# Kernel optimization log

Measured on AMD Instinct MI355X. Metric: run time of the kernel, lower is better.

## Reference

```python
import jax, jax.numpy as jnp
import numpy as np

B, T, F_IN = 64, 512, 264        # batch, time, total features
NONLSTM = 8                      # trailing non-LSTM feature channels
F_LSTM = F_IN - NONLSTM          # 256 features fed to the LSTM stack
HIDDEN = [512, 512]              # stacked OptimizedLSTMCell dims
DENSE = [512, 256]
PRED, FPP = 16, 4                # predictions, features_per_prediction


def _glorot(key, shape):
    fan_in, fan_out = shape[0], shape[1]
    lim = jnp.sqrt(6.0 / (fan_in + fan_out))
    return jax.random.uniform(key, shape, jnp.float32, -lim, lim)


def setup_inputs() -> dict:
    key = jax.random.key(0)
    ks = jax.random.split(key, 16)
    inp = {"x": jax.random.normal(ks[0], (B, T, F_IN), jnp.float32)}
    # LSTM layer params: Wi [in,4H] (no bias on input proj), Wh [H,4H], b [4H]
    in_dim = F_LSTM
    for j, h in enumerate(HIDDEN):
        inp[f"Wi{j}"] = _glorot(ks[1 + 3 * j], (in_dim, 4 * h))
        inp[f"Wh{j}"] = _glorot(ks[2 + 3 * j], (h, 4 * h))
        inp[f"b{j}"] = jnp.zeros((4 * h,), jnp.float32)
        in_dim = h
    # Dense head
    d_in = HIDDEN[-1] + NONLSTM
    for i, d in enumerate(DENSE):
        inp[f"Wd{i}"] = _glorot(ks[8 + 2 * i], (d_in, d))
        inp[f"bd{i}"] = jnp.zeros((d,), jnp.float32)
        d_in = d
    inp["Wf"] = _glorot(ks[14], (d_in, PRED * FPP))
    inp["bf"] = jnp.zeros((PRED * FPP,), jnp.float32)
    return inp


def lstm_layer(x, Wi, Wh, b):
    """flax OptimizedLSTMCell scanned over time. x: [B, T, F] -> [B, T, H]."""
    Bq = x.shape[0]
    H = Wh.shape[0]
    xw = jnp.einsum('btf,fg->btg', x, Wi)  # precompute input projections

    def step(carry, z_in):
        c, h = carry
        z = z_in + h @ Wh + b
        i, f, g, o = jnp.split(z, 4, axis=-1)
        c = jax.nn.sigmoid(f) * c + jax.nn.sigmoid(i) * jnp.tanh(g)
        h = jax.nn.sigmoid(o) * jnp.tanh(c)
        return (c, h), h

    c0 = jnp.zeros((Bq, H), x.dtype)
    h0 = jnp.zeros((Bq, H), x.dtype)
    _, hs = jax.lax.scan(step, (c0, h0), jnp.swapaxes(xw, 0, 1))
    return jnp.swapaxes(hs, 0, 1)


def reference(x, Wi0, Wh0, b0, Wi1, Wh1, b1, Wd0, bd0, Wd1, bd1, Wf, bf):
    last_features = x[:, -1, -NONLSTM:]          # [B, 8]
    h = x[:, :, :-NONLSTM]                       # [B, T, 256]
    # single LSTM branch: history == T, downsample == 1
    h = lstm_layer(h, Wi0, Wh0, b0)
    h = lstm_layer(h, Wi1, Wh1, b1)
    out = h[:, -1, :]                            # [B, H]
    out = jnp.concatenate([out, last_features], axis=1)
    out = jax.nn.relu(out @ Wd0 + bd0)
    out = jax.nn.relu(out @ Wd1 + bd1)
    out = out @ Wf + bf
    out = out.reshape((-1, PRED, FPP))
    return jax.nn.sigmoid(out)
```

## Files before the change

### kernel.cpp

```cpp
#include <hip/hip_runtime.h>
#include <hip/hip_bf16.h>

typedef __hip_bfloat16 bf16;
typedef short bf16x8 __attribute__((ext_vector_type(8)));
typedef float f32x4 __attribute__((ext_vector_type(4)));
typedef unsigned long long u64;
typedef unsigned int u32;

#define MFMA16(A, B, C) __builtin_amdgcn_mfma_f32_16x16x32_bf16(A, B, C, 0, 0, 0)

__device__ __forceinline__ float sigf(float x) { return 1.f / (1.f + __expf(-x)); }
__device__ __forceinline__ float tanh_fast(float x) { return 2.f / (1.f + __expf(-2.f * x)) - 1.f; }

__device__ __forceinline__ bf16x8 ld16(const u64* p) {
  u64 lo = __hip_atomic_load(p, __ATOMIC_RELAXED, __HIP_MEMORY_SCOPE_SYSTEM);
  u64 hi = __hip_atomic_load(p + 1, __ATOMIC_RELAXED, __HIP_MEMORY_SCOPE_SYSTEM);
  union { u64 q[2]; bf16x8 v; } u;
  u.q[0] = lo; u.q[1] = hi;
  return u.v;
}

__global__ __launch_bounds__(256) void transpose_k(const float* __restrict__ W,
                                                   bf16* __restrict__ WT,
                                                   int K, int N) {
  __shared__ bf16 tile[32][33];
  const int n0 = blockIdx.x * 32, k0 = blockIdx.y * 32;
  const int c = threadIdx.x & 31, r0 = threadIdx.x >> 5;
  for (int i = 0; i < 4; ++i) {
    int r = r0 + 8 * i;
    tile[r][c] = __float2bfloat16(W[(long)(k0 + r) * N + (n0 + c)]);
  }
  __syncthreads();
  for (int i = 0; i < 4; ++i) {
    int r = r0 + 8 * i;
    WT[(long)(n0 + r) * K + (k0 + c)] = tile[c][r];
  }
}

__device__ __forceinline__ void gather16(const u64* __restrict__ mat, int m, int q,
                                         bf16x8* out) {
#pragma unroll
  for (int i = 0; i < 16; ++i) {
    const int s = i * 4 + q;
    out[i] = ld16(mat + ((long)(s << 6) + m) * 2);
  }
}

__global__ __launch_bounds__(256, 1) void lstm2_fused_k(
    const float* __restrict__ x,
    const bf16* __restrict__ WiT0, const bf16* __restrict__ WhT0,
    const float* __restrict__ bias0,
    const bf16* __restrict__ WiT1, const bf16* __restrict__ WhT1,
    const float* __restrict__ bias1,
    u64* __restrict__ h1D, u64* __restrict__ h2D,
    u32* __restrict__ sent)
{
  __shared__ short Wis[32 * 520];
  __shared__ short Whs[32 * 520];
  __shared__ float zs[32 * 66];
  __shared__ __align__(16) bf16 hstage[64 * 8];

  const int layer = blockIdx.x >> 6;
  const int w = blockIdx.x & 63;
  const int tid = threadIdx.x;
  const int lane = tid & 63;
  const int wv = tid >> 6;
  const int q = lane >> 4;
  const int r = lane & 15;

  const int K_in = layer ? 512 : 256;
  const bf16* WiT = layer ? WiT1 : WiT0;
  const bf16* WhT = layer ? WhT1 : WhT0;
  const float* bias = layer ? bias1 : bias0;
  u32* s0 = sent;
  u32* s1 = sent + 512 * 64;
  u64* hprevD = layer ? h2D : h1D;
  u64* houtD = layer ? h2D : h1D;
  u32* smy = (layer ? s1 : s0);

  for (int idx = tid; idx < 32 * 64; idx += 256) {
    const int j = idx >> 6, kc = idx & 63;
    const int zc = (j >> 3) * 512 + w * 8 + (j & 7);
    *(bf16x8*)(Whs + j * 520 + kc * 8) = *(const bf16x8*)(WhT + (long)zc * 512 + kc * 8);
  }
  const int csh = layer ? 6 : 5;
  const int cmask = (1 << csh) - 1;
  for (int idx = tid; idx < (32 << csh); idx += 256) {
    const int j = idx >> csh, kc = idx & cmask;
    const int zc = (j >> 3) * 512 + w * 8 + (j & 7);
    *(bf16x8*)(Wis + j * 520 + kc * 8) = *(const bf16x8*)(WiT + (long)zc * K_in + kc * 8);
  }

  const int m = wv * 16 + r;
  const short* wi0p = Wis + r * 520;
  const short* wi1p = Wis + (16 + r) * 520;
  const short* wh0p = Whs + r * 520;
  const short* wh1p = Whs + (16 + r) * 520;

  const int gb = tid & 63;
  const int gc0 = tid >> 6;
  float bias_r[2][4];
  for (int s = 0; s < 2; ++s)
    for (int g = 0; g < 4; ++g)
      bias_r[s][g] = bias[g * 512 + w * 8 + gc0 + 4 * s];
  float creg[2] = {0.f, 0.f};

  __syncthreads();

  for (int t = 0; t < 512; ++t) {
    f32x4 acc0 = {0.f, 0.f, 0.f, 0.f};
    f32x4 acc1 = {0.f, 0.f, 0.f, 0.f};

    if (layer == 0) {
      bf16x8 ax[8];
      const float* row = x + ((long)m * 512 + t) * 264;
#pragma unroll
      for (int i = 0; i < 8; ++i) {
        const float4 f0 = *(const float4*)(row + i * 32 + q * 8);
        const float4 f1 = *(const float4*)(row + i * 32 + q * 8 + 4);
        union { short s[8]; bf16x8 v8; } o;
        o.s[0] = __builtin_bit_cast(short, __float2bfloat16(f0.x));
        o.s[1] = __builtin_bit_cast(short, __float2bfloat16(f0.y));
        o.s[2] = __builtin_bit_cast(short, __float2bfloat16(f0.z));
        o.s[3] = __builtin_bit_cast(short, __float2bfloat16(f0.w));
        o.s[4] = __builtin_bit_cast(short, __float2bfloat16(f1.x));
        o.s[5] = __builtin_bit_cast(short, __float2bfloat16(f1.y));
        o.s[6] = __builtin_bit_cast(short, __float2bfloat16(f1.z));
        o.s[7] = __builtin_bit_cast(short, __float2bfloat16(f1.w));
        ax[i] = o.v8;
      }
#pragma unroll
      for (int i = 0; i < 8; ++i) {
        const int kk = i * 32;
        acc0 = MFMA16(ax[i], *(const bf16x8*)(wi0p + kk + q * 8), acc0);
        acc1 = MFMA16(ax[i], *(const bf16x8*)(wi1p + kk + q * 8), acc1);
      }
      if (t > 0) {
        if (tid < 64) {
          const u32* sp = s0 + (t - 1) * 64 + tid;
          while (__ballot(__hip_atomic_load(sp, __ATOMIC_RELAXED,
                                            __HIP_MEMORY_SCOPE_SYSTEM) != 0) != ~0ull)
            __builtin_amdgcn_s_sleep(2);
        }
        __syncthreads();
        bf16x8 ah[16];
        gather16(h1D + (long)(t - 1) * 8192, m, q, ah);
#pragma unroll
        for (int i = 0; i < 16; ++i) {
          const int kk = i * 32;
          acc0 = MFMA16(ah[i], *(const bf16x8*)(wh0p + kk + q * 8), acc0);
          acc1 = MFMA16(ah[i], *(const bf16x8*)(wh1p + kk + q * 8), acc1);
        }
      }
    } else {
      if (tid < 64) {
        const u32* sp = s0 + t * 64 + tid;
        while (__ballot(__hip_atomic_load(sp, __ATOMIC_RELAXED,
                                          __HIP_MEMORY_SCOPE_SYSTEM) != 0) != ~0ull)
          __builtin_amdgcn_s_sleep(2);
      }
      __syncthreads();
      bf16x8 ax[16];
      gather16(h1D + (long)t * 8192, m, q, ax);
#pragma unroll
      for (int i = 0; i < 16; ++i) {
        const int kk = i * 32;
        acc0 = MFMA16(ax[i], *(const bf16x8*)(wi0p + kk + q * 8), acc0);
        acc1 = MFMA16(ax[i], *(const bf16x8*)(wi1p + kk + q * 8), acc1);
      }
      if (t > 0) {
        if (tid < 64) {
          const u32* sp = s1 + (t - 1) * 64 + tid;
          while (__ballot(__hip_atomic_load(sp, __ATOMIC_RELAXED,
                                            __HIP_MEMORY_SCOPE_SYSTEM) != 0) != ~0ull)
            __builtin_amdgcn_s_sleep(2);
        }
        __syncthreads();
        bf16x8 ah[16];
        gather16(h2D + (long)(t - 1) * 8192, m, q, ah);
#pragma unroll
        for (int i = 0; i < 16; ++i) {
          const int kk = i * 32;
          acc0 = MFMA16(ah[i], *(const bf16x8*)(wh0p + kk + q * 8), acc0);
          acc1 = MFMA16(ah[i], *(const bf16x8*)(wh1p + kk + q * 8), acc1);
        }
      }
    }

    {
      const int brow = wv * 16 + q * 4;
      for (int i = 0; i < 4; ++i) zs[r * 66 + brow + i] = acc0[i];
      for (int i = 0; i < 4; ++i) zs[(16 + r) * 66 + brow + i] = acc1[i];
    }
    __syncthreads();

    for (int s = 0; s < 2; ++s) {
      const int c = gc0 + 4 * s;
      const float zi = zs[(c)*66 + gb] + bias_r[s][0];
      const float zf = zs[(8 + c) * 66 + gb] + bias_r[s][1];
      const float zg = zs[(16 + c) * 66 + gb] + bias_r[s][2];
      const float zo = zs[(24 + c) * 66 + gb] + bias_r[s][3];
      const float cnew = sigf(zf) * creg[s] + sigf(zi) * tanh_fast(zg);
      const float hnew = sigf(zo) * tanh_fast(cnew);
      creg[s] = cnew;
      hstage[gb * 8 + c] = __float2bfloat16(hnew);
    }
    __syncthreads();

    if (tid < 64) {
      const u64* src = (const u64*)(hstage + tid * 8);
      u64* dst = houtD + (((long)t * 64 + w) * 64 + tid) * 2;
      __hip_atomic_store(dst, src[0], __ATOMIC_RELAXED, __HIP_MEMORY_SCOPE_SYSTEM);
      __hip_atomic_store(dst + 1, src[1], __ATOMIC_RELAXED, __HIP_MEMORY_SCOPE_SYSTEM);
    }
    if (tid == 0)
      __hip_atomic_store(smy + t * 64 + w, 1u, __ATOMIC_RELEASE, __HIP_MEMORY_SCOPE_AGENT);
  }
}

__global__ __launch_bounds__(256) void head_k(
    const u64* __restrict__ h2D,
    const float* __restrict__ x,
    const float* __restrict__ Wd0, const float* __restrict__ bd0,
    const float* __restrict__ Wd1, const float* __restrict__ bd1,
    const float* __restrict__ Wf, const float* __restrict__ bfv,
    float* __restrict__ out) {
  const int b = blockIdx.x, tid = threadIdx.x;
  __shared__ float in0[520];
  __shared__ float d0s[512];
  __shared__ float d1s[256];
  if (tid < 64) {
    const int s = tid;
    bf16x8 v = ld16(h2D + (((long)511 * 64 + s) * 64 + b) * 2);
    union { bf16x8 v8; short sh[8]; } u;
    u.v8 = v;
    for (int j = 0; j < 8; ++j)
      in0[s * 8 + j] = __bfloat162float(__builtin_bit_cast(bf16, u.sh[j]));
  }
  if (tid < 8) in0[512 + tid] = x[((long)(b * 512 + 511)) * 264 + 256 + tid];
  __syncthreads();
  for (int j = tid; j < 512; j += 256) {
    float a = bd0[j];
    for (int k = 0; k < 520; ++k) a += in0[k] * Wd0[(long)k * 512 + j];
    d0s[j] = fmaxf(a, 0.f);
  }
  __syncthreads();
  if (tid < 256) {
    const int j = tid;
    float a = bd1[j];
    for (int k = 0; k < 512; ++k) a += d0s[k] * Wd1[(long)k * 256 + j];
    d1s[j] = fmaxf(a, 0.f);
  }
  __syncthreads();
  if (tid < 64) {
    const int j = tid;
    float a = bfv[j];
    for (int k = 0; k < 256; ++k) a += d1s[k] * Wf[(long)k * 64 + j];
    out[b * 64 + j] = sigf(a);
  }
}

extern "C" void kernel_launch(void* const* d_in, const int* in_sizes, int n_in,
                              void* d_out, int out_size, void* d_ws, size_t ws_size,
                              hipStream_t stream) {
  const float* x   = (const float*)d_in[0];
  const float* Wi0 = (const float*)d_in[1];
  const float* Wh0 = (const float*)d_in[2];
  const float* b0  = (const float*)d_in[3];
  const float* Wi1 = (const float*)d_in[4];
  const float* Wh1 = (const float*)d_in[5];
  const float* b1  = (const float*)d_in[6];
  const float* Wd0 = (const float*)d_in[7];
  const float* bd0 = (const float*)d_in[8];
  const float* Wd1 = (const float*)d_in[9];
  const float* bd1 = (const float*)d_in[10];
  const float* Wf  = (const float*)d_in[11];
  const float* bf_ = (const float*)d_in[12];
  float* out = (float*)d_out;

  char* ws = (char*)d_ws;
  size_t off = 0;
  auto carve = [&](size_t bytes) {
    void* p = ws + off;
    off += (bytes + 255) & ~(size_t)255;
    return p;
  };
  u32* sent = (u32*)carve((size_t)2 * 512 * 64 * 4);
  const size_t zero_bytes = off;
  bf16* WiT0 = (bf16*)carve((size_t)2048 * 256 * 2);
  bf16* WhT0 = (bf16*)carve((size_t)2048 * 512 * 2);
  bf16* WiT1 = (bf16*)carve((size_t)2048 * 512 * 2);
  bf16* WhT1 = (bf16*)carve((size_t)2048 * 512 * 2);
  u64*  h1D  = (u64*)carve((size_t)512 * 64 * 64 * 16);
  u64*  h2D  = (u64*)carve((size_t)512 * 64 * 64 * 16);

  hipMemsetAsync(sent, 0, zero_bytes, stream);

  transpose_k<<<dim3(2048 / 32, 256 / 32), 256, 0, stream>>>(Wi0, WiT0, 256, 2048);
  transpose_k<<<dim3(2048 / 32, 512 / 32), 256, 0, stream>>>(Wh0, WhT0, 512, 2048);
  transpose_k<<<dim3(2048 / 32, 512 / 32), 256, 0, stream>>>(Wi1, WiT1, 512, 2048);
  transpose_k<<<dim3(2048 / 32, 512 / 32), 256, 0, stream>>>(Wh1, WhT1, 512, 2048);

  lstm2_fused_k<<<128, 256, 0, stream>>>(x, WiT0, WhT0, b0, WiT1, WhT1, b1,
                                         h1D, h2D, sent);

  head_k<<<64, 256, 0, stream>>>(h2D, x, Wd0, bd0, Wd1, bd1, Wf, bf_, out);
}
```

Baseline: 2.961 ms.

## Tag hidden-state words with timestep and compute gates directly from MFMA registers

Each bf16 hidden value is now stored as a 32-bit word paired with a timestep tag. Consumers spin on the gathered data itself until every tag matches, instead of relying on release-ordered flags plus separate data stores. The gate nonlinearities run straight from the MFMA accumulators using lane shuffles, which drops the LDS staging buffers and two block barriers per step. Layer-2 outputs go to a 64-slot ring buffer. The cost is doubled h traffic and polling of whole data vectors, and the correctness now depends on the tags.

```diff
diff --git a/kernel.cpp b/kernel.cpp
--- a/kernel.cpp
+++ b/kernel.cpp
@@ -8,17 +8,11 @@
 typedef unsigned int u32;
 
 #define MFMA16(A, B, C) __builtin_amdgcn_mfma_f32_16x16x32_bf16(A, B, C, 0, 0, 0)
+#define LD_SYS(p) __hip_atomic_load((p), __ATOMIC_RELAXED, __HIP_MEMORY_SCOPE_SYSTEM)
+#define ST_SYS(p, v) __hip_atomic_store((p), (v), __ATOMIC_RELAXED, __HIP_MEMORY_SCOPE_SYSTEM)
 
 __device__ __forceinline__ float sigf(float x) { return 1.f / (1.f + __expf(-x)); }
 __device__ __forceinline__ float tanh_fast(float x) { return 2.f / (1.f + __expf(-2.f * x)) - 1.f; }
-
-__device__ __forceinline__ bf16x8 ld16(const u64* p) {
-  u64 lo = __hip_atomic_load(p, __ATOMIC_RELAXED, __HIP_MEMORY_SCOPE_SYSTEM);
-  u64 hi = __hip_atomic_load(p + 1, __ATOMIC_RELAXED, __HIP_MEMORY_SCOPE_SYSTEM);
-  union { u64 q[2]; bf16x8 v; } u;
-  u.q[0] = lo; u.q[1] = hi;
-  return u.v;
-}
 
 __global__ __launch_bounds__(256) void transpose_k(const float* __restrict__ W,
                                                    bf16* __restrict__ WT,
@@ -37,12 +31,41 @@
   }
 }
 
-__device__ __forceinline__ void gather16(const u64* __restrict__ mat, int m, int q,
-                                         bf16x8* out) {
+__device__ __forceinline__ void gather16t(const u64* __restrict__ mat, int m, int q,
+                                          u32 tag, bf16x8* out) {
+  const u64 want = ((u64)tag) | ((u64)tag << 32);
+  const u64* base = mat + (long)m * 4;
+  u64 v[16][4];
 #pragma unroll
   for (int i = 0; i < 16; ++i) {
     const int s = i * 4 + q;
-    out[i] = ld16(mat + ((long)(s << 6) + m) * 2);
+#pragma unroll
+    for (int j = 0; j < 4; ++j) v[i][j] = LD_SYS(base + s * 256 + j);
+  }
+  for (;;) {
+    u64 bad = 0;
+#pragma unroll
+    for (int i = 0; i < 16; ++i)
+#pragma unroll
+      for (int j = 0; j < 4; ++j) bad |= (v[i][j] ^ want) & 0x0000ffff0000ffffULL;
+    if (bad == 0) break;
+    __builtin_amdgcn_s_sleep(1);
+#pragma unroll
+    for (int i = 0; i < 16; ++i) {
+      const int s = i * 4 + q;
+#pragma unroll
+      for (int j = 0; j < 4; ++j) v[i][j] = LD_SYS(base + s * 256 + j);
+    }
+  }
+#pragma unroll
+  for (int i = 0; i < 16; ++i) {
+    union { u32 u[4]; bf16x8 v8; } o;
+#pragma unroll
+    for (int j = 0; j < 4; ++j) {
+      const u32 lo = (u32)v[i][j], hi = (u32)(v[i][j] >> 32);
+      o.u[j] = (lo >> 16) | (hi & 0xffff0000u);
+    }
+    out[i] = o.v8;
   }
 }
 
@@ -52,13 +75,11 @@
     const float* __restrict__ bias0,
     const bf16* __restrict__ WiT1, const bf16* __restrict__ WhT1,
     const float* __restrict__ bias1,
-    u64* __restrict__ h1D, u64* __restrict__ h2D,
+    u64* __restrict__ h1T, u64* __restrict__ h2R,
     u32* __restrict__ sent)
 {
   __shared__ short Wis[32 * 520];
   __shared__ short Whs[32 * 520];
-  __shared__ float zs[32 * 66];
-  __shared__ __align__(16) bf16 hstage[64 * 8];
 
   const int layer = blockIdx.x >> 6;
   const int w = blockIdx.x & 63;
@@ -74,9 +95,7 @@
   const float* bias = layer ? bias1 : bias0;
   u32* s0 = sent;
   u32* s1 = sent + 512 * 64;
-  u64* hprevD = layer ? h2D : h1D;
-  u64* houtD = layer ? h2D : h1D;
-  u32* smy = (layer ? s1 : s0);
+  u32* outR32 = (u32*)(layer ? h2R : h1T);
 
   for (int idx = tid; idx < 32 * 64; idx += 256) {
     const int j = idx >> 6, kc = idx & 63;
@@ -97,13 +116,11 @@
   const short* wh0p = Whs + r * 520;
   const short* wh1p = Whs + (16 + r) * 520;
 
-  const int gb = tid & 63;
-  const int gc0 = tid >> 6;
-  float bias_r[2][4];
-  for (int s = 0; s < 2; ++s)
-    for (int g = 0; g < 4; ++g)
-      bias_r[s][g] = bias[g * 512 + w * 8 + gc0 + 4 * s];
-  float creg[2] = {0.f, 0.f};
+  const float bi_i = bias[0 * 512 + w * 8 + (r & 7)];
+  const float bi_f = bias[1 * 512 + w * 8 + (r & 7)];
+  const float bi_g = bias[2 * 512 + w * 8 + (r & 7)];
+  const float bi_o = bias[3 * 512 + w * 8 + (r & 7)];
+  float creg[4] = {0.f, 0.f, 0.f, 0.f};
 
   __syncthreads();
 
@@ -138,13 +155,11 @@
       if (t > 0) {
         if (tid < 64) {
           const u32* sp = s0 + (t - 1) * 64 + tid;
-          while (__ballot(__hip_atomic_load(sp, __ATOMIC_RELAXED,
-                                            __HIP_MEMORY_SCOPE_SYSTEM) != 0) != ~0ull)
-            __builtin_amdgcn_s_sleep(2);
+          while (__ballot(LD_SYS(sp) == (u32)t) != ~0ull) __builtin_amdgcn_s_sleep(1);
         }
         __syncthreads();
         bf16x8 ah[16];
-        gather16(h1D + (long)(t - 1) * 8192, m, q, ah);
+        gather16t(h1T + (long)(t - 1) * 16384, m, q, (u32)t, ah);
 #pragma unroll
         for (int i = 0; i < 16; ++i) {
           const int kk = i * 32;
@@ -155,13 +170,11 @@
     } else {
       if (tid < 64) {
         const u32* sp = s0 + t * 64 + tid;
-        while (__ballot(__hip_atomic_load(sp, __ATOMIC_RELAXED,
-                                          __HIP_MEMORY_SCOPE_SYSTEM) != 0) != ~0ull)
-          __builtin_amdgcn_s_sleep(2);
+        while (__ballot(LD_SYS(sp) == (u32)(t + 1)) != ~0ull) __builtin_amdgcn_s_sleep(1);
       }
       __syncthreads();
       bf16x8 ax[16];
-      gather16(h1D + (long)t * 8192, m, q, ax);
+      gather16t(h1T + (long)t * 16384, m, q, (u32)(t + 1), ax);
 #pragma unroll
       for (int i = 0; i < 16; ++i) {
         const int kk = i * 32;
@@ -171,13 +184,11 @@
       if (t > 0) {
         if (tid < 64) {
           const u32* sp = s1 + (t - 1) * 64 + tid;
-          while (__ballot(__hip_atomic_load(sp, __ATOMIC_RELAXED,
-                                            __HIP_MEMORY_SCOPE_SYSTEM) != 0) != ~0ull)
-            __builtin_amdgcn_s_sleep(2);
+          while (__ballot(LD_SYS(sp) == (u32)t) != ~0ull) __builtin_amdgcn_s_sleep(1);
         }
         __syncthreads();
         bf16x8 ah[16];
-        gather16(h2D + (long)(t - 1) * 8192, m, q, ah);
+        gather16t(h2R + (long)((t - 1) & 63) * 16384, m, q, (u32)t, ah);
 #pragma unroll
         for (int i = 0; i < 16; ++i) {
           const int kk = i * 32;
@@ -187,39 +198,34 @@
       }
     }
 
-    {
-      const int brow = wv * 16 + q * 4;
-      for (int i = 0; i < 4; ++i) zs[r * 66 + brow + i] = acc0[i];
-      for (int i = 0; i < 4; ++i) zs[(16 + r) * 66 + brow + i] = acc1[i];
-    }
-    __syncthreads();
-
-    for (int s = 0; s < 2; ++s) {
-      const int c = gc0 + 4 * s;
-      const float zi = zs[(c)*66 + gb] + bias_r[s][0];
-      const float zf = zs[(8 + c) * 66 + gb] + bias_r[s][1];
-      const float zg = zs[(16 + c) * 66 + gb] + bias_r[s][2];
-      const float zo = zs[(24 + c) * 66 + gb] + bias_r[s][3];
-      const float cnew = sigf(zf) * creg[s] + sigf(zi) * tanh_fast(zg);
-      const float hnew = sigf(zo) * tanh_fast(cnew);
-      creg[s] = cnew;
-      hstage[gb * 8 + c] = __float2bfloat16(hnew);
-    }
-    __syncthreads();
-
-    if (tid < 64) {
-      const u64* src = (const u64*)(hstage + tid * 8);
-      u64* dst = houtD + (((long)t * 64 + w) * 64 + tid) * 2;
-      __hip_atomic_store(dst, src[0], __ATOMIC_RELAXED, __HIP_MEMORY_SCOPE_SYSTEM);
-      __hip_atomic_store(dst + 1, src[1], __ATOMIC_RELAXED, __HIP_MEMORY_SCOPE_SYSTEM);
-    }
-    if (tid == 0)
-      __hip_atomic_store(smy + t * 64 + w, 1u, __ATOMIC_RELEASE, __HIP_MEMORY_SCOPE_AGENT);
+    f32x4 zfv, zov;
+#pragma unroll
+    for (int i = 0; i < 4; ++i) {
+      zfv[i] = __shfl_xor(acc0[i], 8);
+      zov[i] = __shfl_xor(acc1[i], 8);
+    }
+    if (r < 8) {
+      const long slotw = layer ? (long)(t & 63) * 32768 : (long)t * 32768;
+      u32* dst = outR32 + slotw + ((w * 64 + wv * 16 + q * 4) * 8 + r);
+#pragma unroll
+      for (int i = 0; i < 4; ++i) {
+        const float zi = acc0[i] + bi_i;
+        const float zf = zfv[i] + bi_f;
+        const float zg = acc1[i] + bi_g;
+        const float zo = zov[i] + bi_o;
+        const float cnew = sigf(zf) * creg[i] + sigf(zi) * tanh_fast(zg);
+        const float hnew = sigf(zo) * tanh_fast(cnew);
+        creg[i] = cnew;
+        const u32 hb = (u32)__builtin_bit_cast(unsigned short, __float2bfloat16(hnew));
+        ST_SYS(dst + i * 8, (hb << 16) | (u32)(t + 1));
+      }
+    }
+    if (tid == 0) ST_SYS(sent + (layer * 512 + t) * 64 + w, (u32)(t + 1));
   }
 }
 
 __global__ __launch_bounds__(256) void head_k(
-    const u64* __restrict__ h2D,
+    const u64* __restrict__ h2R,
     const float* __restrict__ x,
     const float* __restrict__ Wd0, const float* __restrict__ bd0,
     const float* __restrict__ Wd1, const float* __restrict__ bd1,
@@ -231,11 +237,14 @@
   __shared__ float d1s[256];
   if (tid < 64) {
     const int s = tid;
-    bf16x8 v = ld16(h2D + (((long)511 * 64 + s) * 64 + b) * 2);
-    union { bf16x8 v8; short sh[8]; } u;
-    u.v8 = v;
-    for (int j = 0; j < 8; ++j)
-      in0[s * 8 + j] = __bfloat162float(__builtin_bit_cast(bf16, u.sh[j]));
+    const u64* base = h2R + (long)63 * 16384 + ((long)s * 64 + b) * 4;
+    for (int j = 0; j < 4; ++j) {
+      const u64 v = LD_SYS(base + j);
+      const unsigned short p0 = (unsigned short)((u32)v >> 16);
+      const unsigned short p1 = (unsigned short)((u32)(v >> 32) >> 16);
+      in0[s * 8 + 2 * j] = __bfloat162float(__builtin_bit_cast(bf16, p0));
+      in0[s * 8 + 2 * j + 1] = __bfloat162float(__builtin_bit_cast(bf16, p1));
+    }
   }
   if (tid < 8) in0[512 + tid] = x[((long)(b * 512 + 511)) * 264 + 256 + tid];
   __syncthreads();
@@ -291,8 +300,8 @@
   bf16* WhT0 = (bf16*)carve((size_t)2048 * 512 * 2);
   bf16* WiT1 = (bf16*)carve((size_t)2048 * 512 * 2);
   bf16* WhT1 = (bf16*)carve((size_t)2048 * 512 * 2);
-  u64*  h1D  = (u64*)carve((size_t)512 * 64 * 64 * 16);
-  u64*  h2D  = (u64*)carve((size_t)512 * 64 * 64 * 16);
+  u64*  h1T  = (u64*)carve((size_t)512 * 64 * 64 * 32);
+  u64*  h2R  = (u64*)carve((size_t)64 * 64 * 64 * 32);
 
   hipMemsetAsync(sent, 0, zero_bytes, stream);
 
@@ -302,7 +311,7 @@
   transpose_k<<<dim3(2048 / 32, 512 / 32), 256, 0, stream>>>(Wh1, WhT1, 512, 2048);
 
   lstm2_fused_k<<<128, 256, 0, stream>>>(x, WiT0, WhT0, b0, WiT1, WhT1, b1,
-                                         h1D, h2D, sent);
-
-  head_k<<<64, 256, 0, stream>>>(h2D, x, Wd0, bd0, Wd1, bd1, Wf, bf_, out);
-}
+                                         h1T, h2R, sent);
+
+  head_k<<<64, 256, 0, stream>>>(h2R, x, Wd0, bd0, Wd1, bd1, Wf, bf_, out);
+}
```

Measured after the change: 6.107 ms. +106.2%, slower.
